# Kernel optimization log

Hardware: AMD Instinct MI355X
Metric: run time of the kernel (lower is better)

The kernel has to match this reference:

```python
import jax, jax.numpy as jnp
import numpy as np

B, INPUT_DIM, N = 8, 1, 4096
DIM, DEPTH, HEADS, DIM_HEAD = 512, 4, 8, 64
WINDOW = 128
NUM_CLASSES = 10
INNER = int(DIM * 4 * 2 / 3)  # 1365 (GEGLU FeedForward inner dim)
LN_EPS = 1e-5


def setup_inputs() -> dict:
    key = jax.random.key(0)
    ks = jax.random.split(key, 12)
    s = 0.02
    inner_qkv = HEADS * DIM_HEAD
    return {
        "x": jax.random.normal(ks[0], (B, INPUT_DIM, N), dtype=jnp.float32),
        "lin_emb_w": jax.random.normal(ks[1], (DIM, INPUT_DIM), dtype=jnp.float32) * s,
        "lin_emb_b": jnp.zeros((DIM,), dtype=jnp.float32),
        "qkv_w": jax.random.normal(ks[2], (DEPTH, 3 * inner_qkv, DIM), dtype=jnp.float32) * s,
        "out_w": jax.random.normal(ks[3], (DEPTH, DIM, inner_qkv), dtype=jnp.float32) * s,
        "ff_ln_g": jnp.ones((DEPTH, DIM), dtype=jnp.float32),
        "ff_ln_b": jnp.zeros((DEPTH, DIM), dtype=jnp.float32),
        "ff_w1": jax.random.normal(ks[4], (DEPTH, 2 * INNER, DIM), dtype=jnp.float32) * s,
        "ff_w2": jax.random.normal(ks[5], (DEPTH, DIM, INNER), dtype=jnp.float32) * s,
        "proj_w": jax.random.normal(ks[6], (NUM_CLASSES, DIM), dtype=jnp.float32) * s,
        "proj_b": jnp.zeros((NUM_CLASSES,), dtype=jnp.float32),
    }


def _layer_norm(x, g, b):
    mu = jnp.mean(x, axis=-1, keepdims=True)
    var = jnp.mean(jnp.square(x - mu), axis=-1, keepdims=True)
    return (x - mu) * jax.lax.rsqrt(var + LN_EPS) * g + b


def _local_attention(q, k, v, w):
    # q,k,v: (b, h, n, d). Non-causal sliding window: each window of size w
    # attends to windows [i-1, i, i+1] (look_backward=1, look_forward=1),
    # with out-of-range key positions masked (lucidrains LocalAttention,
    # autopad=True, exact_windowsize=False). n is a multiple of w here.
    b, h, n, d = q.shape
    nw = n // w
    scale = d ** -0.5
    qw = q.reshape(b, h, nw, w, d) * scale
    kw = k.reshape(b, h, nw, w, d)
    vw = v.reshape(b, h, nw, w, d)

    def look_around(t):  # (b,h,nw,w,d) -> (b,h,nw,3w,d)
        tp = jnp.pad(t, ((0, 0), (0, 0), (1, 1), (0, 0), (0, 0)))
        return jnp.concatenate([tp[:, :, i:i + nw] for i in range(3)], axis=3)

    k3 = look_around(kw)
    v3 = look_around(vw)

    # validity mask for boundary windows (fake keys from padding)
    win = jnp.arange(nw)
    kpos = (win[:, None] - 1) * w + jnp.arange(3 * w)[None, :]  # (nw, 3w)
    valid = (kpos >= 0) & (kpos < n)

    scores = jnp.einsum('bhnqd,bhnkd->bhnqk', qw, k3)  # (b,h,nw,w,3w)
    scores = jnp.where(valid[None, None, :, None, :], scores,
                       jnp.finfo(scores.dtype).min)
    attn = jax.nn.softmax(scores, axis=-1)
    out = jnp.einsum('bhnqk,bhnkd->bhnqd', attn, v3)
    return out.reshape(b, h, n, d)


def reference(x, lin_emb_w, lin_emb_b, qkv_w, out_w, ff_ln_g, ff_ln_b,
              ff_w1, ff_w2, proj_w, proj_b):
    b = x.shape[0]
    h = jnp.einsum('bdn,ed->bne', x, lin_emb_w) + lin_emb_b  # (b, n, dim)
    for l in range(DEPTH):
        # --- LocalMHA (no prenorm) + residual ---
        qkv = jnp.einsum('bnd,ed->bne', h, qkv_w[l])
        q, k, v = jnp.split(qkv, 3, axis=-1)
        def heads(t):
            return t.reshape(b, N, HEADS, DIM_HEAD).transpose(0, 2, 1, 3)
        o = _local_attention(heads(q), heads(k), heads(v), WINDOW)
        o = o.transpose(0, 2, 1, 3).reshape(b, N, HEADS * DIM_HEAD)
        h = jnp.einsum('bne,de->bnd', o, out_w[l]) + h
        # --- GEGLU FeedForward (prenorm inside) + residual ---
        y = _layer_norm(h, ff_ln_g[l], ff_ln_b[l])
        y = jnp.einsum('bnd,ed->bne', y, ff_w1[l])
        u, gate = jnp.split(y, 2, axis=-1)
        y = u * jax.nn.gelu(gate, approximate=False)
        h = h + jnp.einsum('bne,de->bnd', y, ff_w2[l])
    pooled = h.mean(axis=1)  # mean_pooling
    return pooled @ proj_w.T + proj_b
```

## Files before the change

kernel.cpp:

```cpp
#include <hip/hip_runtime.h>
#include <hip/hip_bf16.h>
#include <math.h>

typedef __attribute__((ext_vector_type(8))) short short8;
typedef __attribute__((ext_vector_type(4))) float f32x4;

#define MFMA16 __builtin_amdgcn_mfma_f32_16x16x32_bf16
#define GLOAD(dst, src) __builtin_amdgcn_global_load_lds( \
    (const __attribute__((address_space(1))) void*)(src), \
    (__attribute__((address_space(3))) void*)(dst), 16, 0, 0)

__device__ __forceinline__ short f2bf(float f){
  unsigned u = __float_as_uint(f);
  u = (u + 0x7FFFu + ((u >> 16) & 1u)) >> 16;
  return (short)u;
}

__device__ __forceinline__ size_t pidx(int r, int k, int K){
  return ((size_t)((r >> 8) * (K >> 5) + (k >> 5)) * 256 + (r & 255)) * 32 + (k & 31);
}

__device__ __forceinline__ float gelu_phi(float g){
  float ax = fabsf(g) * 0.70710678118f;
  float t  = 1.f / (1.f + 0.3275911f * ax);
  float pp = ((((1.061405429f * t - 1.453152027f) * t + 1.421413741f) * t
               - 0.284496736f) * t + 0.254829592f) * t;
  float e  = 1.f - pp * __expf(-ax * ax);
  return 0.5f + copysignf(0.5f, g) * e;
}

__global__ void cast_pack_kernel(const float* __restrict__ s, short* __restrict__ d,
                                 int NROW, int K){
  int i = blockIdx.x * 256 + threadIdx.x;
  int per = NROW * K;
  int l = i / per, rem = i - l * per;
  int r = rem / K, c = rem - r * K;
  d[(size_t)l * per + pidx(r, c, K)] = f2bf(s[i]);
}

__global__ void w1p_kernel(const float* __restrict__ s, short* __restrict__ d){
  int i = blockIdx.x * 256 + threadIdx.x;
  int c  = i & 511;
  int rl = i >> 9;
  int r  = rl % 2816;
  int l  = rl / 2816;
  int g  = r >> 5, sfx = r & 31;
  int j  = g * 16 + (sfx & 15);
  float v = 0.f;
  if (j < 1365){
    int sr = (sfx < 16) ? j : 1365 + j;
    v = s[((size_t)l * 2730 + sr) * 512 + c];
  }
  d[(size_t)l * 2816 * 512 + pidx(r, c, 512)] = f2bf(v);
}

__global__ void w2p_kernel(const float* __restrict__ s, short* __restrict__ d){
  int i = blockIdx.x * 256 + threadIdx.x;
  int c = i % 1408;
  int rr = i / 1408;
  int l = rr >> 9, row = rr & 511;
  float v = (c < 1365) ? s[(size_t)rr * 1365 + c] : 0.f;
  d[(size_t)l * 512 * 1408 + pidx(row, c, 1408)] = f2bf(v);
}

__global__ void embed_kernel(const float* __restrict__ x, const float* __restrict__ w,
                             const float* __restrict__ bias, float* __restrict__ hf,
                             short* __restrict__ hb){
  long i = ((long)blockIdx.x * 256 + threadIdx.x) * 8;
  long row = i >> 9; int e = (int)(i & 511);
  float xv = x[row];
  float4 w0 = *(const float4*)(w + e),    w1 = *(const float4*)(w + e + 4);
  float4 b0 = *(const float4*)(bias + e), b1 = *(const float4*)(bias + e + 4);
  float4 o0, o1;
  o0.x = xv*w0.x+b0.x; o0.y = xv*w0.y+b0.y; o0.z = xv*w0.z+b0.z; o0.w = xv*w0.w+b0.w;
  o1.x = xv*w1.x+b1.x; o1.y = xv*w1.y+b1.y; o1.z = xv*w1.z+b1.z; o1.w = xv*w1.w+b1.w;
  *(float4*)(hf + i) = o0; *(float4*)(hf + i + 4) = o1;
  short8 hv;
  hv[0]=f2bf(o0.x); hv[1]=f2bf(o0.y); hv[2]=f2bf(o0.z); hv[3]=f2bf(o0.w);
  hv[4]=f2bf(o1.x); hv[5]=f2bf(o1.y); hv[6]=f2bf(o1.z); hv[7]=f2bf(o1.w);
  *(short8*)(hb + pidx((int)row, e, 512)) = hv;
}

template<int EPI>
__global__ __launch_bounds__(1024, 4)
void gemm_pk(const short* __restrict__ A, const short* __restrict__ B, int K,
             float* __restrict__ Cres, short* __restrict__ Cbf, int ldcb)
{
  __shared__ short As[4][256][32];
  __shared__ short Bs[4][256][32];
  char* smA = (char*)As; char* smB = (char*)Bs;
  const int tid = threadIdx.x, lane = tid & 63, w = tid >> 6;
  const int wm = w >> 2, wn = w & 3;
  const int NT = K >> 5;
  const int nwg = gridDim.x * gridDim.y;
  const int f = blockIdx.y * gridDim.x + blockIdx.x;
  const int sw = (f & 7) * (nwg >> 3) + (f >> 3);
  const long tm = (long)(sw / gridDim.x) * 256;
  const long tn = (long)(sw % gridDim.x) * 256;

  const int srow = tid >> 2;
  const int sc   = (tid & 3) ^ ((srow >> 1) & 3);
  const short* aS = A + ((size_t)(tm >> 8) * NT * 256 + srow) * 32 + sc * 8;
  const short* bS = B + ((size_t)(tn >> 8) * NT * 256 + srow) * 32 + sc * 8;
  const int ldsW = w * 1024;

  f32x4 acc[4][4];
  #pragma unroll
  for (int i = 0; i < 4; i++)
    #pragma unroll
    for (int j = 0; j < 4; j++) acc[i][j] = (f32x4){0.f,0.f,0.f,0.f};

  const int rA = wm * 64 + (lane & 15);
  const int rB = wn * 64 + (lane & 15);
  const int abase = rA * 64 + (((lane >> 4) ^ ((rA >> 1) & 3)) * 16);
  const int bbase = rB * 64 + (((lane >> 4) ^ ((rB >> 1) & 3)) * 16);

  GLOAD(smA + 0 + ldsW, aS);             GLOAD(smB + 0 + ldsW, bS);
  GLOAD(smA + 16384 + ldsW, aS + 8192);  GLOAD(smB + 16384 + ldsW, bS + 8192);
  GLOAD(smA + 32768 + ldsW, aS + 16384); GLOAD(smB + 32768 + ldsW, bS + 16384);
  asm volatile("s_waitcnt vmcnt(4)" ::: "memory");
  __builtin_amdgcn_s_barrier();

  for (int t = 0; t < NT; ++t){
    const int cur = (t & 3) * 16384;
    const int stb = ((t + 3) & 3) * 16384;
    const size_t ko = (size_t)(t + 3) * 8192;
    if (t + 3 < NT){ GLOAD(smA + stb + ldsW, aS + ko); GLOAD(smB + stb + ldsW, bS + ko); }
    short8 a[4], bb[4];
    #pragma unroll
    for (int ni = 0; ni < 4; ni++)
      bb[ni] = *(const short8*)(smB + cur + bbase + ni * 1024);
    #pragma unroll
    for (int q = 0; q < 4; q++)
      a[q] = *(const short8*)(smA + cur + abase + q * 1024);
    #pragma unroll
    for (int q = 0; q < 4; q++)
      #pragma unroll
      for (int ni = 0; ni < 4; ni++)
        acc[q][ni] = MFMA16(a[q], bb[ni], acc[q][ni], 0, 0, 0);
    if      (t + 3 < NT) asm volatile("s_waitcnt vmcnt(4)" ::: "memory");
    else if (t + 2 < NT) asm volatile("s_waitcnt vmcnt(2)" ::: "memory");
    else if (t + 1 < NT) asm volatile("s_waitcnt vmcnt(0)" ::: "memory");
    __builtin_amdgcn_s_barrier();
  }

  #pragma unroll
  for (int mi = 0; mi < 4; mi++){
    if (EPI == 3){
      #pragma unroll
      for (int p = 0; p < 2; p++)
        #pragma unroll
        for (int v = 0; v < 4; v++){
          int row = (int)(tm + wm * 64 + mi * 16 + (lane >> 4) * 4 + v);
          int col = (int)((tn >> 1) + wn * 32 + p * 16 + (lane & 15));
          float u = acc[mi][2*p][v], g = acc[mi][2*p+1][v];
          Cbf[pidx(row, col, 1408)] = f2bf(u * g * gelu_phi(g));
        }
    } else {
      #pragma unroll
      for (int ni = 0; ni < 4; ni++)
        #pragma unroll
        for (int v = 0; v < 4; v++){
          int row = (int)(tm + wm * 64 + mi * 16 + (lane >> 4) * 4 + v);
          int col = (int)(tn + wn * 64 + ni * 16 + (lane & 15));
          float x = acc[mi][ni][v];
          if (EPI == 0) Cbf[(long)row * ldcb + col] = f2bf(x);
          else if (EPI == 1) Cres[(long)row * 512 + col] = x + Cres[(long)row * 512 + col];
          else { float rr = x + Cres[(long)row * 512 + col];
                 Cres[(long)row * 512 + col] = rr;
                 Cbf[pidx(row, col, 512)] = f2bf(rr); }
        }
    }
  }
}

__global__ __launch_bounds__(256, 2)
void attn_kernel(const short* __restrict__ qkv, short* __restrict__ o)
{
  __shared__ short Ks[128 * 64];
  __shared__ short Vt[64 * 136];
  __shared__ short Ps[4 * 32 * 128];
  const int win = blockIdx.x, hh = blockIdx.y, b = blockIdx.z;
  const int tid = threadIdx.x, lane = tid & 63, w = tid >> 6;
  const long qrow0 = (long)b * 4096 + (long)win * 128;

  short8 qf[2][2];
  #pragma unroll
  for (int i = 0; i < 2; i++)
    #pragma unroll
    for (int kk = 0; kk < 2; kk++)
      qf[i][kk] = *(const short8*)(qkv + (qrow0 + w * 32 + i * 16 + (lane & 15)) * 1536
                                   + hh * 64 + kk * 32 + (lane >> 4) * 8);

  f32x4 oacc[2][4];
  #pragma unroll
  for (int i = 0; i < 2; i++)
    #pragma unroll
    for (int j = 0; j < 4; j++) oacc[i][j] = (f32x4){0.f,0.f,0.f,0.f};
  float rs[2][4];
  #pragma unroll
  for (int i = 0; i < 2; i++)
    #pragma unroll
    for (int v = 0; v < 4; v++) rs[i][v] = 0.f;

  const int row_s = tid >> 3, c_s = tid & 7;
  for (int cc = 0; cc < 3; cc++){
    int kw = win - 1 + cc;
    if (kw < 0 || kw >= 32) continue;
    const long krow0 = (long)b * 4096 + (long)kw * 128;
    __syncthreads();
    #pragma unroll
    for (int r = 0; r < 4; r++){
      int row = row_s + r * 32;
      const short* src = qkv + (krow0 + row) * 1536 + hh * 64;
      short8 kv = *(const short8*)(src + 512 + c_s * 8);
      *(short8*)((char*)Ks + ((row * 128 + c_s * 16) ^ ((row & 7) << 4))) = kv;
      short8 vv = *(const short8*)(src + 1024 + c_s * 8);
      #pragma unroll
      for (int e = 0; e < 8; e++) Vt[(c_s * 8 + e) * 136 + row] = vv[e];
    }
    __syncthreads();

    f32x4 sacc[2][8];
    #pragma unroll
    for (int i = 0; i < 2; i++)
      #pragma unroll
      for (int j = 0; j < 8; j++) sacc[i][j] = (f32x4){0.f,0.f,0.f,0.f};
    #pragma unroll
    for (int kk = 0; kk < 2; kk++){
      short8 bbk[8];
      int ac = (kk * 32 + (lane >> 4) * 8) * 2;
      #pragma unroll
      for (int j = 0; j < 8; j++){
        int br = j * 16 + (lane & 15);
        bbk[j] = *(const short8*)((char*)Ks + ((br * 128 + ac) ^ ((br & 7) << 4)));
      }
      #pragma unroll
      for (int i = 0; i < 2; i++)
        #pragma unroll
        for (int j = 0; j < 8; j++)
          sacc[i][j] = MFMA16(qf[i][kk], bbk[j], sacc[i][j], 0, 0, 0);
    }

    short* myPs = Ps + w * 32 * 128;
    float psum[2][4];
    #pragma unroll
    for (int i = 0; i < 2; i++)
      #pragma unroll
      for (int v = 0; v < 4; v++) psum[i][v] = 0.f;
    #pragma unroll
    for (int i = 0; i < 2; i++)
      #pragma unroll
      for (int j = 0; j < 8; j++)
        #pragma unroll
        for (int v = 0; v < 4; v++){
          float p = expf(0.125f * sacc[i][j][v]);
          psum[i][v] += p;
          int prow = i * 16 + (lane >> 4) * 4 + v;
          int pcb  = (j * 16 + (lane & 15)) * 2;
          *(short*)((char*)myPs + ((prow * 256 + pcb) ^ ((prow & 7) << 4))) = f2bf(p);
        }
    #pragma unroll
    for (int i = 0; i < 2; i++)
      #pragma unroll
      for (int v = 0; v < 4; v++){
        float s = psum[i][v];
        s += __shfl_xor(s, 1); s += __shfl_xor(s, 2);
        s += __shfl_xor(s, 4); s += __shfl_xor(s, 8);
        rs[i][v] += s;
      }
    __syncthreads();

    #pragma unroll
    for (int kk = 0; kk < 4; kk++){
      short8 pa[2], vb[4];
      int kb = (kk * 32 + (lane >> 4) * 8) * 2;
      #pragma unroll
      for (int i = 0; i < 2; i++){
        int pr = i * 16 + (lane & 15);
        pa[i] = *(const short8*)((char*)myPs + ((pr * 256 + kb) ^ ((pr & 7) << 4)));
      }
      #pragma unroll
      for (int j = 0; j < 4; j++){
        int vr = j * 16 + (lane & 15);
        vb[j] = *(const short8*)((char*)Vt + (vr * 272 + kb));
      }
      #pragma unroll
      for (int i = 0; i < 2; i++)
        #pragma unroll
        for (int j = 0; j < 4; j++)
          oacc[i][j] = MFMA16(pa[i], vb[j], oacc[i][j], 0, 0, 0);
    }
  }

  #pragma unroll
  for (int i = 0; i < 2; i++)
    #pragma unroll
    for (int j = 0; j < 4; j++)
      #pragma unroll
      for (int v = 0; v < 4; v++){
        int row = (int)(qrow0 + w * 32 + i * 16 + (lane >> 4) * 4 + v);
        int col = hh * 64 + j * 16 + (lane & 15);
        o[pidx(row, col, 512)] = f2bf(oacc[i][j][v] / rs[i][v]);
      }
}

__global__ __launch_bounds__(256)
void ln_kernel(const float* __restrict__ h, const float* __restrict__ g,
               const float* __restrict__ be, short* __restrict__ y)
{
  long row = (long)blockIdx.x * 4 + (threadIdx.x >> 6);
  int lane = threadIdx.x & 63;
  const float* x = h + row * 512 + lane * 8;
  float4 a0 = *(const float4*)x;
  float4 a1 = *(const float4*)(x + 4);
  float v[8] = {a0.x, a0.y, a0.z, a0.w, a1.x, a1.y, a1.z, a1.w};
  float s = 0.f, sq = 0.f;
  #pragma unroll
  for (int j = 0; j < 8; j++){ s += v[j]; sq += v[j] * v[j]; }
  #pragma unroll
  for (int m = 1; m <= 32; m <<= 1){ s += __shfl_xor(s, m); sq += __shfl_xor(sq, m); }
  float mu = s * (1.f / 512.f);
  float var = sq * (1.f / 512.f) - mu * mu;
  float rstd = rsqrtf(var + 1e-5f);
  short8 yv;
  #pragma unroll
  for (int j = 0; j < 8; j++){
    int c = lane * 8 + j;
    yv[j] = f2bf((v[j] - mu) * rstd * g[c] + be[c]);
  }
  *(short8*)(y + pidx((int)row, lane * 8, 512)) = yv;
}

__global__ void pool_partial(const float* __restrict__ h, float* __restrict__ part){
  int b = blockIdx.x, ch = blockIdx.y, t = threadIdx.x;
  float s0 = 0.f, s1 = 0.f;
  const float* base = h + ((long)b * 4096 + ch * 128) * 512;
  for (int n = 0; n < 128; n++){
    s0 += base[(long)n * 512 + t];
    s1 += base[(long)n * 512 + t + 256];
  }
  part[((b * 32 + ch) * 512) + t] = s0;
  part[((b * 32 + ch) * 512) + t + 256] = s1;
}

__global__ void pool_proj(const float* __restrict__ part, const float* __restrict__ pw,
                          const float* __restrict__ pb, float* __restrict__ out){
  __shared__ float pooled[512];
  __shared__ float red[4];
  int b = blockIdx.x, t = threadIdx.x;
  int lane = t & 63, w = t >> 6;
  float s0 = 0.f, s1 = 0.f;
  for (int ch = 0; ch < 32; ch++){
    s0 += part[((b * 32 + ch) * 512) + t];
    s1 += part[((b * 32 + ch) * 512) + t + 256];
  }
  pooled[t] = s0 * (1.f / 4096.f);
  pooled[t + 256] = s1 * (1.f / 4096.f);
  __syncthreads();
  for (int cls = 0; cls < 10; cls++){
    float p = pooled[t] * pw[cls * 512 + t] + pooled[t + 256] * pw[cls * 512 + t + 256];
    p += __shfl_xor(p, 1); p += __shfl_xor(p, 2); p += __shfl_xor(p, 4);
    p += __shfl_xor(p, 8); p += __shfl_xor(p, 16); p += __shfl_xor(p, 32);
    if (lane == 0) red[w] = p;
    __syncthreads();
    if (t == 0) out[b * 10 + cls] = red[0] + red[1] + red[2] + red[3] + pb[cls];
    __syncthreads();
  }
}

extern "C" void kernel_launch(void* const* d_in, const int* in_sizes, int n_in,
                              void* d_out, int out_size, void* d_ws, size_t ws_size,
                              hipStream_t stream)
{
  const float* x      = (const float*)d_in[0];
  const float* lin_w  = (const float*)d_in[1];
  const float* lin_b  = (const float*)d_in[2];
  const float* qkvw_f = (const float*)d_in[3];
  const float* outw_f = (const float*)d_in[4];
  const float* lng    = (const float*)d_in[5];
  const float* lnb    = (const float*)d_in[6];
  const float* w1_f   = (const float*)d_in[7];
  const float* w2_f   = (const float*)d_in[8];
  const float* projw  = (const float*)d_in[9];
  const float* projb  = (const float*)d_in[10];
  float* out = (float*)d_out;

  char* ws = (char*)d_ws;
  float* hf32 = (float*)(ws);
  short* abuf = (short*)(ws + 67108864);
  short* qkvb = (short*)(ws + 100663296);
  short* gbuf = qkvb;
  short* obuf = (short*)(ws + 201326592);
  float* part = (float*)(ws + 234881024);
  short* wqkv = (short*)(ws + 235405312);
  short* wout = (short*)(ws + 247988224);
  short* w1p  = (short*)(ws + 250085376);
  short* w2p  = (short*)(ws + 261619712);

  cast_pack_kernel<<<12288, 256, 0, stream>>>(qkvw_f, wqkv, 1536, 512);
  cast_pack_kernel<<<4096, 256, 0, stream>>>(outw_f, wout, 512, 512);
  w1p_kernel<<<22528, 256, 0, stream>>>(w1_f, w1p);
  w2p_kernel<<<11264, 256, 0, stream>>>(w2_f, w2p);
  embed_kernel<<<8192, 256, 0, stream>>>(x, lin_w, lin_b, hf32, abuf);

  for (int l = 0; l < 4; l++){
    gemm_pk<0><<<dim3(6, 128), 1024, 0, stream>>>(abuf, wqkv + (size_t)l * 1536 * 512, 512,
                                                  nullptr, qkvb, 1536);
    attn_kernel<<<dim3(32, 8, 8), 256, 0, stream>>>(qkvb, obuf);
    gemm_pk<1><<<dim3(2, 128), 1024, 0, stream>>>(obuf, wout + (size_t)l * 512 * 512, 512,
                                                  hf32, nullptr, 0);
    ln_kernel<<<8192, 256, 0, stream>>>(hf32, lng + l * 512, lnb + l * 512, abuf);
    gemm_pk<3><<<dim3(11, 128), 1024, 0, stream>>>(abuf, w1p + (size_t)l * 2816 * 512, 512,
                                                   nullptr, gbuf, 1408);
    gemm_pk<2><<<dim3(2, 128), 1024, 0, stream>>>(gbuf, w2p + (size_t)l * 512 * 1408, 1408,
                                                  hf32, abuf, 512);
  }
  pool_partial<<<dim3(8, 32), 256, 0, stream>>>(hf32, part);
  pool_proj<<<8, 256, 0, stream>>>(part, projw, projb, out);
}
```

Before: 1.904 ms.

## Store QKV head-major and stream K tiles into LDS via async global loads

The QKV GEMM epilogue now writes Q, K and V in a head-major [head][row][64] layout instead of row-major with a 1536 stride, so the attention kernel reads contiguous 128-byte rows per head. The K tile is then loaded straight into shared memory with global_load_lds, with the XOR swizzle applied on the source-address side. The softmax exponent also switches to the fast __expf intrinsic. The trade-off is scattered GEMM epilogue stores in exchange for coalesced attention loads, plus slightly lower exp precision.

```diff
diff --git a/kernel.cpp b/kernel.cpp
--- a/kernel.cpp
+++ b/kernel.cpp
@@ -164,11 +164,16 @@
           int row = (int)(tm + wm * 64 + mi * 16 + (lane >> 4) * 4 + v);
           int col = (int)(tn + wn * 64 + ni * 16 + (lane & 15));
           float x = acc[mi][ni][v];
-          if (EPI == 0) Cbf[(long)row * ldcb + col] = f2bf(x);
-          else if (EPI == 1) Cres[(long)row * 512 + col] = x + Cres[(long)row * 512 + col];
-          else { float rr = x + Cres[(long)row * 512 + col];
-                 Cres[(long)row * 512 + col] = rr;
-                 Cbf[pidx(row, col, 512)] = f2bf(rr); }
+          if (EPI == 4){
+            int hd = col >> 6, d = col & 63;
+            Cbf[((size_t)hd * 32768 + row) * 64 + d] = f2bf(x);
+          } else if (EPI == 1){
+            Cres[(long)row * 512 + col] = x + Cres[(long)row * 512 + col];
+          } else {
+            float rr = x + Cres[(long)row * 512 + col];
+            Cres[(long)row * 512 + col] = rr;
+            Cbf[pidx(row, col, 512)] = f2bf(rr);
+          }
         }
     }
   }
@@ -180,17 +185,21 @@
   __shared__ short Ks[128 * 64];
   __shared__ short Vt[64 * 136];
   __shared__ short Ps[4 * 32 * 128];
+  char* smK = (char*)Ks;
   const int win = blockIdx.x, hh = blockIdx.y, b = blockIdx.z;
   const int tid = threadIdx.x, lane = tid & 63, w = tid >> 6;
   const long qrow0 = (long)b * 4096 + (long)win * 128;
+  const short* Qb = qkv + (size_t)hh * 2097152;
+  const short* Kb = qkv + (size_t)(8 + hh) * 2097152;
+  const short* Vb = qkv + (size_t)(16 + hh) * 2097152;
 
   short8 qf[2][2];
   #pragma unroll
   for (int i = 0; i < 2; i++)
     #pragma unroll
     for (int kk = 0; kk < 2; kk++)
-      qf[i][kk] = *(const short8*)(qkv + (qrow0 + w * 32 + i * 16 + (lane & 15)) * 1536
-                                   + hh * 64 + kk * 32 + (lane >> 4) * 8);
+      qf[i][kk] = *(const short8*)(Qb + (qrow0 + w * 32 + i * 16 + (lane & 15)) * 64
+                                   + kk * 32 + (lane >> 4) * 8);
 
   f32x4 oacc[2][4];
   #pragma unroll
@@ -203,19 +212,21 @@
     #pragma unroll
     for (int v = 0; v < 4; v++) rs[i][v] = 0.f;
 
-  const int row_s = tid >> 3, c_s = tid & 7;
+  const int row_s = tid >> 3;
+  const int c_s   = tid & 7;
+  const int schK  = (tid & 7) ^ ((tid >> 3) & 7);
   for (int cc = 0; cc < 3; cc++){
     int kw = win - 1 + cc;
     if (kw < 0 || kw >= 32) continue;
     const long krow0 = (long)b * 4096 + (long)kw * 128;
     __syncthreads();
+    const short* srcK = Kb + (krow0 + row_s) * 64 + schK * 8;
+    const short* srcV = Vb + (krow0 + row_s) * 64 + c_s * 8;
     #pragma unroll
     for (int r = 0; r < 4; r++){
+      GLOAD(smK + w * 1024 + r * 4096, srcK + (size_t)r * 32 * 64);
+      short8 vv = *(const short8*)(srcV + (size_t)r * 32 * 64);
       int row = row_s + r * 32;
-      const short* src = qkv + (krow0 + row) * 1536 + hh * 64;
-      short8 kv = *(const short8*)(src + 512 + c_s * 8);
-      *(short8*)((char*)Ks + ((row * 128 + c_s * 16) ^ ((row & 7) << 4))) = kv;
-      short8 vv = *(const short8*)(src + 1024 + c_s * 8);
       #pragma unroll
       for (int e = 0; e < 8; e++) Vt[(c_s * 8 + e) * 136 + row] = vv[e];
     }
@@ -254,7 +265,7 @@
       for (int j = 0; j < 8; j++)
         #pragma unroll
         for (int v = 0; v < 4; v++){
-          float p = expf(0.125f * sacc[i][j][v]);
+          float p = __expf(0.125f * sacc[i][j][v]);
           psum[i][v] += p;
           int prow = i * 16 + (lane >> 4) * 4 + v;
           int pcb  = (j * 16 + (lane & 15)) * 2;
@@ -405,8 +416,8 @@
   embed_kernel<<<8192, 256, 0, stream>>>(x, lin_w, lin_b, hf32, abuf);
 
   for (int l = 0; l < 4; l++){
-    gemm_pk<0><<<dim3(6, 128), 1024, 0, stream>>>(abuf, wqkv + (size_t)l * 1536 * 512, 512,
-                                                  nullptr, qkvb, 1536);
+    gemm_pk<4><<<dim3(6, 128), 1024, 0, stream>>>(abuf, wqkv + (size_t)l * 1536 * 512, 512,
+                                                  nullptr, qkvb, 0);
     attn_kernel<<<dim3(32, 8, 8), 256, 0, stream>>>(qkvb, obuf);
     gemm_pk<1><<<dim3(2, 128), 1024, 0, stream>>>(obuf, wout + (size_t)l * 512 * 512, 512,
                                                   hf32, nullptr, 0);
```

Measured after the change: 1.803 ms. 5.3% less time.
